# Optimization experiments

Measured on AMD Instinct MI355X. Metric: run time of the kernel, lower is better.

The kernel has to match this reference:

```python
import jax, jax.numpy as jnp
import numpy as np

D_MODEL = 1024
HEAD_SIZE = 64

def setup_inputs() -> dict:
    key = jax.random.key(0)
    ks = jax.random.split(key, 7)
    s = 1.0 / np.sqrt(D_MODEL)
    x = jax.random.normal(ks[0], (4, 4096, D_MODEL), dtype=jnp.float32)
    Wq = jax.random.uniform(ks[1], (D_MODEL, HEAD_SIZE), jnp.float32, -s, s)
    bq = jax.random.uniform(ks[2], (HEAD_SIZE,), jnp.float32, -s, s)
    Wk = jax.random.uniform(ks[3], (D_MODEL, HEAD_SIZE), jnp.float32, -s, s)
    bk = jax.random.uniform(ks[4], (HEAD_SIZE,), jnp.float32, -s, s)
    Wv = jax.random.uniform(ks[5], (D_MODEL, HEAD_SIZE), jnp.float32, -s, s)
    bv = jax.random.uniform(ks[6], (HEAD_SIZE,), jnp.float32, -s, s)
    return {"x": x, "Wq": Wq, "bq": bq, "Wk": Wk, "bk": bk, "Wv": Wv, "bv": bv}

def reference(x, Wq, bq, Wk, bk, Wv, bv):
    # x: [B, S, D]; projections to [B, S, H]
    Q = jnp.einsum('bsd,dh->bsh', x, Wq) + bq
    K = jnp.einsum('bsd,dh->bsh', x, Wk) + bk
    V = jnp.einsum('bsd,dh->bsh', x, Wv) + bv
    scores = jnp.einsum('bqh,bkh->bqk', Q, K) / jnp.sqrt(jnp.float32(HEAD_SIZE))
    attn = jax.nn.softmax(scores, axis=-1)  # [B, S, S]
    return jnp.einsum('bqk,bkh->bqh', attn, V)
```

## Files before the change

kernel.cpp:

```cpp
#include <hip/hip_runtime.h>
#include <hip/hip_bf16.h>


#define S_LEN 4096
#define D_MODEL 1024

typedef __attribute__((ext_vector_type(8))) short bf16x8;
typedef __attribute__((ext_vector_type(4))) float f32x4;
typedef __attribute__((ext_vector_type(16))) float f32x16;

__device__ inline short f2bf(float f) {
    union { float f; unsigned u; } v;
    v.f = f;
    unsigned r = v.u + 0x7fffu + ((v.u >> 16) & 1u);
    return (short)(r >> 16);
}

__device__ inline unsigned cvt_pk(float lo, float hi) {
    unsigned r;
    asm("v_cvt_pk_bf16_f32 %0, %1, %2" : "=v"(r) : "v"(lo), "v"(hi));
    return r;
}

__device__ inline void pl32swap(unsigned& a, unsigned& b) {
    asm("v_permlane32_swap_b32 %0, %1" : "+v"(a), "+v"(b));
}

__device__ inline f32x16 fzero16() {
    f32x16 z;
#pragma unroll
    for (int i = 0; i < 16; ++i) z[i] = 0.f;
    return z;
}

__device__ inline void gload_lds16(const void* g, void* l) {
    __builtin_amdgcn_global_load_lds((const __attribute__((address_space(1))) void*)g,
                                     (__attribute__((address_space(3))) void*)l, 16, 0, 0);
}

__global__ void prep_w(const float* __restrict__ Wq, const float* __restrict__ Wk,
                       const float* __restrict__ Wv, short* __restrict__ WtF) {
    int idx = blockIdx.x * 256 + threadIdx.x;
    int j = idx & 7;
    int lane = (idx >> 3) & 63;
    int f = idx >> 9;
    int ntg = f % 12;
    int kb = f / 12;
    int k = (kb >> 1) * 64 + (kb & 1) * 32 + (lane >> 4) * 8 + j;
    int c = ntg * 16 + (lane & 15);
    const float* W = (c < 64) ? Wq : (c < 128 ? Wk : Wv);
    WtF[idx] = f2bf(W[k * 64 + (c & 63)]);
}

__launch_bounds__(512)
__global__ void proj_kernel(const float* __restrict__ x, const short* __restrict__ WtF,
                            const float* __restrict__ bq, const float* __restrict__ bk,
                            const float* __restrict__ bv,
                            short* __restrict__ Qb, short* __restrict__ Kb,
                            short* __restrict__ Vt) {
    __shared__ __align__(16) char smem[73728];
    const float CEXP = 0.18033688011112042f;
    int w = threadIdx.x >> 6;
    int lane = threadIdx.x & 63;
    int g = lane >> 4, ln = lane & 15;
    int rt = w >> 2, nh = w & 3;
    int rowbase = blockIdx.x * 32;

    char* xbuf = smem;
    char* wbuf = smem + 24576;
    const char* xB = (const char*)x;
    const char* WtB = (const char*)WtF;

    auto stageX = [&](int buf, int bkt) {
        int od = w * 1024 + lane * 16;
        int row = od >> 8, col = od & 255;
        const char* src = xB + (size_t)(rowbase + row) * 4096 + bkt * 256
                          + (col ^ ((row & 7) << 5));
        gload_lds16(src, xbuf + buf * 8192 + w * 1024);
    };
    auto stageW = [&](int buf, int bkt) {
#pragma unroll
        for (int i = 0; i < 3; ++i) {
            const char* src = WtB + (size_t)bkt * 24576 + w * 3072 + i * 1024 + lane * 16;
            gload_lds16(src, wbuf + buf * 24576 + w * 3072 + i * 1024);
        }
    };

    f32x4 acc[3];
#pragma unroll
    for (int i = 0; i < 3; ++i) acc[i] = (f32x4){0.f, 0.f, 0.f, 0.f};

    stageX(0, 0);
    stageW(0, 0);
    stageX(1, 1);

    int arow = rt * 16 + ln;
    int aswz = (arow & 7) << 5;

#pragma unroll 1
    for (int t = 0; t < 16; ++t) {
        asm volatile("s_waitcnt vmcnt(1)" ::: "memory");
        __builtin_amdgcn_s_barrier();
        __builtin_amdgcn_sched_barrier(0);
        {
            int tn1 = t + 1 > 15 ? 15 : t + 1;
            int tn2 = t + 2 > 15 ? 15 : t + 2;
            stageW((t + 1) & 1, tn1);
            int xs = t + 2; while (xs >= 3) xs -= 3;
            stageX(xs, tn2);
        }
        int xj = t; while (xj >= 3) xj -= 3;
        const char* xc = xbuf + xj * 8192;
        const char* wc = wbuf + (t & 1) * 24576;

#pragma unroll
        for (int kk = 0; kk < 2; ++kk) {
            int cb = (kk * 128 + g * 32) ^ aswz;
            f32x4 X0 = *(const f32x4*)(xc + arow * 256 + cb);
            f32x4 X1 = *(const f32x4*)(xc + arow * 256 + cb + 16);
            union { bf16x8 v; unsigned u[4]; } A;
            A.u[0] = cvt_pk(X0[0], X0[1]);
            A.u[1] = cvt_pk(X0[2], X0[3]);
            A.u[2] = cvt_pk(X1[0], X1[1]);
            A.u[3] = cvt_pk(X1[2], X1[3]);
#pragma unroll
            for (int j = 0; j < 3; ++j) {
                int fr = kk * 12 + nh * 3 + j;
                bf16x8 bfr = *(const bf16x8*)(wc + fr * 1024 + lane * 16);
                acc[j] = __builtin_amdgcn_mfma_f32_16x16x32_bf16(A.v, bfr, acc[j], 0, 0, 0);
            }
        }
    }

    __syncthreads();
    short* vsm = (short*)smem;
#pragma unroll
    for (int j = 0; j < 3; ++j) {
        int ntg = nh * 3 + j;
        int c = ntg * 16 + ln;
        int proj = ntg >> 2;
        int h = c & 63;
        float bias = (proj == 0 ? bq : (proj == 1 ? bk : bv))[h];
#pragma unroll
        for (int r = 0; r < 4; ++r) {
            int srow = rowbase + rt * 16 + g * 4 + r;
            float v = acc[j][r] + bias;
            if (proj == 0) v *= CEXP;
            short hv = f2bf(v);
            if (proj == 0) {
                Qb[(size_t)srow * 64 + h] = hv;
            } else if (proj == 1) {
                Kb[(size_t)srow * 64 + h] = hv;
            } else {
                vsm[h * 36 + rt * 16 + g * 4 + r] = hv;
            }
        }
    }
    __syncthreads();
    {
        int t = threadIdx.x;
        int h = t >> 3, c = t & 7;
        uint2 val = *(const uint2*)(vsm + h * 36 + c * 4);
        int bb = rowbase >> 12;
        int sg = (rowbase & 4095) + c * 4;
        *(uint2*)(Vt + (((size_t)(bb * 64 + h)) << 12) + sg) = val;
    }
}

__launch_bounds__(512)
__global__ void attn_kernel(const short* __restrict__ Qb, const short* __restrict__ Kb,
                            const short* __restrict__ Vt, float* __restrict__ out) {
    __shared__ __align__(16) char smraw[131072];
    __shared__ float lsm[256];
    int lane = threadIdx.x & 63;
    int w = threadIdx.x >> 6;
    int l31 = lane & 31, hi = lane >> 5;
    int sp = w >> 1, qt = w & 1;

    int bid = blockIdx.x;
    int sb = (bid & 7) * 32 + (bid >> 3);
    int b = sb >> 6, qs = sb & 63;
    size_t qrow0 = ((size_t)b << 12) + (size_t)qs * 64;

    char* base = smraw + sp * 32768;
    char* kbuf = base;
    char* vbuf = base + 16384;

    const char* KB = (const char*)(Kb + (((size_t)b << 12) + sp * 1024) * 64);
    const char* VB = (const char*)Vt + (((size_t)b * 64) << 13) + (size_t)sp * 2048;

    auto stageT = [&](int buf, int t) {
        if (qt == 0) {
            char* dst = kbuf + buf * 8192;
#pragma unroll
            for (int i = 0; i < 8; ++i) {
                int od = i * 1024 + lane * 16;
                int row = od >> 7, colb = od & 127;
                const char* src = KB + (size_t)(t * 64 + row) * 128 + (colb ^ ((row & 7) << 4));
                gload_lds16(src, dst + i * 1024);
            }
        } else {
            char* dst = vbuf + buf * 8192;
#pragma unroll
            for (int i = 0; i < 8; ++i) {
                int od = i * 1024 + lane * 16;
                int row = od >> 7, colb = od & 127;
                const char* src = VB + (size_t)row * 8192 + t * 128 + (colb ^ ((row & 7) << 4));
                gload_lds16(src, dst + i * 1024);
            }
        }
    };

    bf16x8 qf[4];
    {
        const short* qp = Qb + (qrow0 + qt * 32 + l31) * 64 + hi * 8;
#pragma unroll
        for (int ks = 0; ks < 4; ++ks) qf[ks] = *(const bf16x8*)(qp + ks * 16);
    }

    f32x16 oacc0 = fzero16(), oacc1 = fzero16();
    float lacc[16];
#pragma unroll
    for (int r = 0; r < 16; ++r) lacc[r] = 0.f;

    int swz = (l31 & 7) << 4;
    stageT(0, 0);

#pragma unroll 1
    for (int t = 0; t < 16; ++t) {
        asm volatile("s_waitcnt vmcnt(0)" ::: "memory");
        __builtin_amdgcn_s_barrier();
        __builtin_amdgcn_sched_barrier(0);
        if (t < 15) stageT((t + 1) & 1, t + 1);

        const char* kc = kbuf + (t & 1) * 8192;
        const char* vc = vbuf + (t & 1) * 8192;

        bf16x8 kf[8];
#pragma unroll
        for (int kt = 0; kt < 2; ++kt)
#pragma unroll
            for (int ks = 0; ks < 4; ++ks)
                kf[kt * 4 + ks] = *(const bf16x8*)(kc + (kt * 32 + l31) * 128
                                                  + ((ks * 32 + hi * 16) ^ swz));
        f32x16 s0 = fzero16(), s1 = fzero16();
#pragma unroll
        for (int ks = 0; ks < 4; ++ks) {
            s0 = __builtin_amdgcn_mfma_f32_32x32x16_bf16(kf[ks], qf[ks], s0, 0, 0, 0);
            s1 = __builtin_amdgcn_mfma_f32_32x32x16_bf16(kf[4 + ks], qf[ks], s1, 0, 0, 0);
        }

        bf16x8 vf[8];
#pragma unroll
        for (int ht = 0; ht < 2; ++ht)
#pragma unroll
            for (int kk = 0; kk < 4; ++kk)
                vf[ht * 4 + kk] = *(const bf16x8*)(vc + (ht * 32 + l31) * 128
                                                   + ((kk * 32 + hi * 16) ^ swz));

        float p0[16], p1[16];
#pragma unroll
        for (int r = 0; r < 16; ++r) p0[r] = exp2f(s0[r]);
#pragma unroll
        for (int r = 0; r < 16; ++r) p1[r] = exp2f(s1[r]);
#pragma unroll
        for (int r = 0; r < 16; ++r) lacc[r] += p0[r] + p1[r];

        union { unsigned u[4]; bf16x8 v; } t00, t01, t10, t11;
        {
            unsigned D[8];
#pragma unroll
            for (int dw = 0; dw < 8; ++dw) D[dw] = cvt_pk(p0[2 * dw], p0[2 * dw + 1]);
            pl32swap(D[0], D[2]); pl32swap(D[1], D[3]);
            pl32swap(D[4], D[6]); pl32swap(D[5], D[7]);
            t00.u[0] = D[0]; t00.u[1] = D[1]; t00.u[2] = D[2]; t00.u[3] = D[3];
            t01.u[0] = D[4]; t01.u[1] = D[5]; t01.u[2] = D[6]; t01.u[3] = D[7];
        }
        {
            unsigned D[8];
#pragma unroll
            for (int dw = 0; dw < 8; ++dw) D[dw] = cvt_pk(p1[2 * dw], p1[2 * dw + 1]);
            pl32swap(D[0], D[2]); pl32swap(D[1], D[3]);
            pl32swap(D[4], D[6]); pl32swap(D[5], D[7]);
            t10.u[0] = D[0]; t10.u[1] = D[1]; t10.u[2] = D[2]; t10.u[3] = D[3];
            t11.u[0] = D[4]; t11.u[1] = D[5]; t11.u[2] = D[6]; t11.u[3] = D[7];
        }

        oacc0 = __builtin_amdgcn_mfma_f32_32x32x16_bf16(vf[0], t00.v, oacc0, 0, 0, 0);
        oacc1 = __builtin_amdgcn_mfma_f32_32x32x16_bf16(vf[4], t00.v, oacc1, 0, 0, 0);
        oacc0 = __builtin_amdgcn_mfma_f32_32x32x16_bf16(vf[1], t01.v, oacc0, 0, 0, 0);
        oacc1 = __builtin_amdgcn_mfma_f32_32x32x16_bf16(vf[5], t01.v, oacc1, 0, 0, 0);
        oacc0 = __builtin_amdgcn_mfma_f32_32x32x16_bf16(vf[2], t10.v, oacc0, 0, 0, 0);
        oacc1 = __builtin_amdgcn_mfma_f32_32x32x16_bf16(vf[6], t10.v, oacc1, 0, 0, 0);
        oacc0 = __builtin_amdgcn_mfma_f32_32x32x16_bf16(vf[3], t11.v, oacc0, 0, 0, 0);
        oacc1 = __builtin_amdgcn_mfma_f32_32x32x16_bf16(vf[7], t11.v, oacc1, 0, 0, 0);
    }

    float lfin;
    {
        float lt[8];
#pragma unroll
        for (int r = 0; r < 8; ++r) lt[r] = lacc[r] + lacc[r + 8];
#pragma unroll
        for (int st = 4; st >= 1; st >>= 1)
#pragma unroll
            for (int r = 0; r < 4; ++r)
                if (r < st) lt[r] += lt[r + st];
        lfin = lt[0] + __shfl_xor(lt[0], 32);
    }

    __syncthreads();
    float* osm = (float*)smraw;
    {
        float* ow = osm + (size_t)(w * 32 + l31) * 68;
#pragma unroll
        for (int r = 0; r < 16; ++r) {
            int h = (r & 3) + 8 * (r >> 2) + 4 * hi;
            ow[h] = oacc0[r];
            ow[32 + h] = oacc1[r];
        }
        if (hi == 0) lsm[w * 32 + l31] = lfin;
    }
    __syncthreads();
    {
        int tq = threadIdx.x >> 3, hb = (threadIdx.x & 7) * 8;
        int qt2 = tq >> 5, ql = tq & 31;
        f32x4 oa = (f32x4){0.f, 0.f, 0.f, 0.f}, ob = (f32x4){0.f, 0.f, 0.f, 0.f};
        float lsum = 0.f;
#pragma unroll
        for (int sp2 = 0; sp2 < 4; ++sp2) {
            int w2 = sp2 * 2 + qt2;
            lsum += lsm[w2 * 32 + ql];
            const float* src = osm + (size_t)(w2 * 32 + ql) * 68 + hb;
            f32x4 x0 = *(const f32x4*)src;
            f32x4 x1 = *(const f32x4*)(src + 4);
#pragma unroll
            for (int j = 0; j < 4; ++j) { oa[j] += x0[j]; ob[j] += x1[j]; }
        }
        float inv = 1.f / lsum;
        f32x4 r0, r1;
#pragma unroll
        for (int j = 0; j < 4; ++j) { r0[j] = oa[j] * inv; r1[j] = ob[j] * inv; }
        float* op = out + (qrow0 + tq) * 64 + hb;
        *(f32x4*)op = r0;
        *(f32x4*)(op + 4) = r1;
    }
}

extern "C" void kernel_launch(void* const* d_in, const int* in_sizes, int n_in,
                              void* d_out, int out_size, void* d_ws, size_t ws_size,
                              hipStream_t stream) {
    const float* x  = (const float*)d_in[0];
    const float* Wq = (const float*)d_in[1];
    const float* bq = (const float*)d_in[2];
    const float* Wk = (const float*)d_in[3];
    const float* bk = (const float*)d_in[4];
    const float* Wv = (const float*)d_in[5];
    const float* bv = (const float*)d_in[6];

    short* ws = (short*)d_ws;
    short* WtF = ws;
    short* Qb = WtF + 192 * 1024;
    short* Kb = Qb + 16384 * 64;
    short* Vt = Kb + 16384 * 64;

    prep_w<<<768, 256, 0, stream>>>(Wq, Wk, Wv, WtF);
    proj_kernel<<<512, 512, 0, stream>>>(x, WtF, bq, bk, bv, Qb, Kb, Vt);
    attn_kernel<<<256, 512, 0, stream>>>(Qb, Kb, Vt, (float*)d_out);
}
```

Measured before the change: 59.35 us.

## Split keys across all eight waves, each wave covering all 64 query rows

Waves no longer pair up as 4 key splits × 2 query tiles. Each of the 8 waves now takes its own 512-key slice and processes both 32-row query tiles, reusing its K and V fragments across the two. Each wave stages its own 32-key K and V tiles, so LDS reads per MFMA drop and the split of staging work between K and V waves goes away. The cost is doubled accumulator registers (four output tiles), a larger LDS reduction buffer, and an 8-way cross-wave sum at the end.

```diff
diff --git a/kernel.cpp b/kernel.cpp
--- a/kernel.cpp
+++ b/kernel.cpp
@@ -170,58 +170,63 @@
 __launch_bounds__(512)
 __global__ void attn_kernel(const short* __restrict__ Qb, const short* __restrict__ Kb,
                             const short* __restrict__ Vt, float* __restrict__ out) {
-    __shared__ __align__(16) char smraw[131072];
-    __shared__ float lsm[256];
+    __shared__ __align__(16) char smraw[139264];
+    __shared__ float lsm[512];
     int lane = threadIdx.x & 63;
     int w = threadIdx.x >> 6;
     int l31 = lane & 31, hi = lane >> 5;
-    int sp = w >> 1, qt = w & 1;
 
     int bid = blockIdx.x;
     int sb = (bid & 7) * 32 + (bid >> 3);
     int b = sb >> 6, qs = sb & 63;
     size_t qrow0 = ((size_t)b << 12) + (size_t)qs * 64;
 
-    char* base = smraw + sp * 32768;
+    char* base = smraw + w * 16384;
     char* kbuf = base;
-    char* vbuf = base + 16384;
-
-    const char* KB = (const char*)(Kb + (((size_t)b << 12) + sp * 1024) * 64);
-    const char* VB = (const char*)Vt + (((size_t)b * 64) << 13) + (size_t)sp * 2048;
+    char* vbuf = base + 8192;
+
+    const char* KB = (const char*)(Kb + (((size_t)b << 12) + w * 512) * 64);
+    const char* VB = (const char*)Vt + (((size_t)b * 64) << 13) + (size_t)w * 1024;
 
     auto stageT = [&](int buf, int t) {
-        if (qt == 0) {
-            char* dst = kbuf + buf * 8192;
-#pragma unroll
-            for (int i = 0; i < 8; ++i) {
+        {
+            char* dst = kbuf + buf * 4096;
+#pragma unroll
+            for (int i = 0; i < 4; ++i) {
                 int od = i * 1024 + lane * 16;
                 int row = od >> 7, colb = od & 127;
-                const char* src = KB + (size_t)(t * 64 + row) * 128 + (colb ^ ((row & 7) << 4));
+                const char* src = KB + (size_t)(t * 32 + row) * 128 + (colb ^ ((row & 7) << 4));
                 gload_lds16(src, dst + i * 1024);
             }
-        } else {
-            char* dst = vbuf + buf * 8192;
-#pragma unroll
-            for (int i = 0; i < 8; ++i) {
+        }
+        {
+            char* dst = vbuf + buf * 4096;
+#pragma unroll
+            for (int i = 0; i < 4; ++i) {
                 int od = i * 1024 + lane * 16;
-                int row = od >> 7, colb = od & 127;
-                const char* src = VB + (size_t)row * 8192 + t * 128 + (colb ^ ((row & 7) << 4));
+                int row = od >> 7;
+                int od2 = (od & 127) ^ ((row & 7) << 4);
+                int half = (od2 >> 6) & 1, colb = od2 & 63;
+                const char* src = VB + (size_t)(row + half * 32) * 8192 + t * 64 + colb;
                 gload_lds16(src, dst + i * 1024);
             }
         }
     };
 
-    bf16x8 qf[4];
+    bf16x8 qf0[4], qf1[4];
     {
-        const short* qp = Qb + (qrow0 + qt * 32 + l31) * 64 + hi * 8;
-#pragma unroll
-        for (int ks = 0; ks < 4; ++ks) qf[ks] = *(const bf16x8*)(qp + ks * 16);
-    }
-
-    f32x16 oacc0 = fzero16(), oacc1 = fzero16();
-    float lacc[16];
-#pragma unroll
-    for (int r = 0; r < 16; ++r) lacc[r] = 0.f;
+        const short* qp0 = Qb + (qrow0 + l31) * 64 + hi * 8;
+        const short* qp1 = Qb + (qrow0 + 32 + l31) * 64 + hi * 8;
+#pragma unroll
+        for (int ks = 0; ks < 4; ++ks) {
+            qf0[ks] = *(const bf16x8*)(qp0 + ks * 16);
+            qf1[ks] = *(const bf16x8*)(qp1 + ks * 16);
+        }
+    }
+
+    f32x16 oacc00 = fzero16(), oacc01 = fzero16();
+    f32x16 oacc10 = fzero16(), oacc11 = fzero16();
+    float lq0 = 0.f, lq1 = 0.f;
 
     int swz = (l31 & 7) << 4;
     stageT(0, 0);
@@ -233,105 +238,117 @@
         __builtin_amdgcn_sched_barrier(0);
         if (t < 15) stageT((t + 1) & 1, t + 1);
 
-        const char* kc = kbuf + (t & 1) * 8192;
-        const char* vc = vbuf + (t & 1) * 8192;
-
-        bf16x8 kf[8];
-#pragma unroll
-        for (int kt = 0; kt < 2; ++kt)
+        const char* kc = kbuf + (t & 1) * 4096;
+        const char* vc = vbuf + (t & 1) * 4096;
+
+        bf16x8 kf[4];
+#pragma unroll
+        for (int ks = 0; ks < 4; ++ks)
+            kf[ks] = *(const bf16x8*)(kc + l31 * 128 + ((ks * 32 + hi * 16) ^ swz));
+        bf16x8 vf[4];
+#pragma unroll
+        for (int ht = 0; ht < 2; ++ht)
+#pragma unroll
+            for (int ks2 = 0; ks2 < 2; ++ks2)
+                vf[ht * 2 + ks2] = *(const bf16x8*)(vc + l31 * 128
+                                    + ((ht * 64 + ks2 * 32 + hi * 16) ^ swz));
+
+        {
+            f32x16 s = fzero16();
 #pragma unroll
             for (int ks = 0; ks < 4; ++ks)
-                kf[kt * 4 + ks] = *(const bf16x8*)(kc + (kt * 32 + l31) * 128
-                                                  + ((ks * 32 + hi * 16) ^ swz));
-        f32x16 s0 = fzero16(), s1 = fzero16();
-#pragma unroll
-        for (int ks = 0; ks < 4; ++ks) {
-            s0 = __builtin_amdgcn_mfma_f32_32x32x16_bf16(kf[ks], qf[ks], s0, 0, 0, 0);
-            s1 = __builtin_amdgcn_mfma_f32_32x32x16_bf16(kf[4 + ks], qf[ks], s1, 0, 0, 0);
-        }
-
-        bf16x8 vf[8];
-#pragma unroll
-        for (int ht = 0; ht < 2; ++ht)
-#pragma unroll
-            for (int kk = 0; kk < 4; ++kk)
-                vf[ht * 4 + kk] = *(const bf16x8*)(vc + (ht * 32 + l31) * 128
-                                                   + ((kk * 32 + hi * 16) ^ swz));
-
-        float p0[16], p1[16];
-#pragma unroll
-        for (int r = 0; r < 16; ++r) p0[r] = exp2f(s0[r]);
-#pragma unroll
-        for (int r = 0; r < 16; ++r) p1[r] = exp2f(s1[r]);
-#pragma unroll
-        for (int r = 0; r < 16; ++r) lacc[r] += p0[r] + p1[r];
-
-        union { unsigned u[4]; bf16x8 v; } t00, t01, t10, t11;
-        {
+                s = __builtin_amdgcn_mfma_f32_32x32x16_bf16(kf[ks], qf0[ks], s, 0, 0, 0);
+            float p[16];
+#pragma unroll
+            for (int r = 0; r < 16; ++r) p[r] = exp2f(s[r]);
+            {
+                float sa[8];
+#pragma unroll
+                for (int r = 0; r < 8; ++r) sa[r] = p[r] + p[r + 8];
+#pragma unroll
+                for (int st = 4; st >= 1; st >>= 1)
+#pragma unroll
+                    for (int r = 0; r < 4; ++r)
+                        if (r < st) sa[r] += sa[r + st];
+                lq0 += sa[0];
+            }
             unsigned D[8];
 #pragma unroll
-            for (int dw = 0; dw < 8; ++dw) D[dw] = cvt_pk(p0[2 * dw], p0[2 * dw + 1]);
+            for (int dw = 0; dw < 8; ++dw) D[dw] = cvt_pk(p[2 * dw], p[2 * dw + 1]);
             pl32swap(D[0], D[2]); pl32swap(D[1], D[3]);
             pl32swap(D[4], D[6]); pl32swap(D[5], D[7]);
-            t00.u[0] = D[0]; t00.u[1] = D[1]; t00.u[2] = D[2]; t00.u[3] = D[3];
-            t01.u[0] = D[4]; t01.u[1] = D[5]; t01.u[2] = D[6]; t01.u[3] = D[7];
-        }
-        {
+            union { unsigned u[4]; bf16x8 v; } t0, t1;
+            t0.u[0] = D[0]; t0.u[1] = D[1]; t0.u[2] = D[2]; t0.u[3] = D[3];
+            t1.u[0] = D[4]; t1.u[1] = D[5]; t1.u[2] = D[6]; t1.u[3] = D[7];
+            oacc00 = __builtin_amdgcn_mfma_f32_32x32x16_bf16(vf[0], t0.v, oacc00, 0, 0, 0);
+            oacc01 = __builtin_amdgcn_mfma_f32_32x32x16_bf16(vf[2], t0.v, oacc01, 0, 0, 0);
+            oacc00 = __builtin_amdgcn_mfma_f32_32x32x16_bf16(vf[1], t1.v, oacc00, 0, 0, 0);
+            oacc01 = __builtin_amdgcn_mfma_f32_32x32x16_bf16(vf[3], t1.v, oacc01, 0, 0, 0);
+        }
+        {
+            f32x16 s = fzero16();
+#pragma unroll
+            for (int ks = 0; ks < 4; ++ks)
+                s = __builtin_amdgcn_mfma_f32_32x32x16_bf16(kf[ks], qf1[ks], s, 0, 0, 0);
+            float p[16];
+#pragma unroll
+            for (int r = 0; r < 16; ++r) p[r] = exp2f(s[r]);
+            {
+                float sa[8];
+#pragma unroll
+                for (int r = 0; r < 8; ++r) sa[r] = p[r] + p[r + 8];
+#pragma unroll
+                for (int st = 4; st >= 1; st >>= 1)
+#pragma unroll
+                    for (int r = 0; r < 4; ++r)
+                        if (r < st) sa[r] += sa[r + st];
+                lq1 += sa[0];
+            }
             unsigned D[8];
 #pragma unroll
-            for (int dw = 0; dw < 8; ++dw) D[dw] = cvt_pk(p1[2 * dw], p1[2 * dw + 1]);
+            for (int dw = 0; dw < 8; ++dw) D[dw] = cvt_pk(p[2 * dw], p[2 * dw + 1]);
             pl32swap(D[0], D[2]); pl32swap(D[1], D[3]);
             pl32swap(D[4], D[6]); pl32swap(D[5], D[7]);
-            t10.u[0] = D[0]; t10.u[1] = D[1]; t10.u[2] = D[2]; t10.u[3] = D[3];
-            t11.u[0] = D[4]; t11.u[1] = D[5]; t11.u[2] = D[6]; t11.u[3] = D[7];
-        }
-
-        oacc0 = __builtin_amdgcn_mfma_f32_32x32x16_bf16(vf[0], t00.v, oacc0, 0, 0, 0);
-        oacc1 = __builtin_amdgcn_mfma_f32_32x32x16_bf16(vf[4], t00.v, oacc1, 0, 0, 0);
-        oacc0 = __builtin_amdgcn_mfma_f32_32x32x16_bf16(vf[1], t01.v, oacc0, 0, 0, 0);
-        oacc1 = __builtin_amdgcn_mfma_f32_32x32x16_bf16(vf[5], t01.v, oacc1, 0, 0, 0);
-        oacc0 = __builtin_amdgcn_mfma_f32_32x32x16_bf16(vf[2], t10.v, oacc0, 0, 0, 0);
-        oacc1 = __builtin_amdgcn_mfma_f32_32x32x16_bf16(vf[6], t10.v, oacc1, 0, 0, 0);
-        oacc0 = __builtin_amdgcn_mfma_f32_32x32x16_bf16(vf[3], t11.v, oacc0, 0, 0, 0);
-        oacc1 = __builtin_amdgcn_mfma_f32_32x32x16_bf16(vf[7], t11.v, oacc1, 0, 0, 0);
-    }
-
-    float lfin;
-    {
-        float lt[8];
-#pragma unroll
-        for (int r = 0; r < 8; ++r) lt[r] = lacc[r] + lacc[r + 8];
-#pragma unroll
-        for (int st = 4; st >= 1; st >>= 1)
-#pragma unroll
-            for (int r = 0; r < 4; ++r)
-                if (r < st) lt[r] += lt[r + st];
-        lfin = lt[0] + __shfl_xor(lt[0], 32);
-    }
+            union { unsigned u[4]; bf16x8 v; } t0, t1;
+            t0.u[0] = D[0]; t0.u[1] = D[1]; t0.u[2] = D[2]; t0.u[3] = D[3];
+            t1.u[0] = D[4]; t1.u[1] = D[5]; t1.u[2] = D[6]; t1.u[3] = D[7];
+            oacc10 = __builtin_amdgcn_mfma_f32_32x32x16_bf16(vf[0], t0.v, oacc10, 0, 0, 0);
+            oacc11 = __builtin_amdgcn_mfma_f32_32x32x16_bf16(vf[2], t0.v, oacc11, 0, 0, 0);
+            oacc10 = __builtin_amdgcn_mfma_f32_32x32x16_bf16(vf[1], t1.v, oacc10, 0, 0, 0);
+            oacc11 = __builtin_amdgcn_mfma_f32_32x32x16_bf16(vf[3], t1.v, oacc11, 0, 0, 0);
+        }
+    }
+
+    float lf0 = lq0 + __shfl_xor(lq0, 32);
+    float lf1 = lq1 + __shfl_xor(lq1, 32);
 
     __syncthreads();
     float* osm = (float*)smraw;
     {
-        float* ow = osm + (size_t)(w * 32 + l31) * 68;
+        float* ow0 = osm + (size_t)(w * 64 + l31) * 68;
+        float* ow1 = osm + (size_t)(w * 64 + 32 + l31) * 68;
 #pragma unroll
         for (int r = 0; r < 16; ++r) {
             int h = (r & 3) + 8 * (r >> 2) + 4 * hi;
-            ow[h] = oacc0[r];
-            ow[32 + h] = oacc1[r];
-        }
-        if (hi == 0) lsm[w * 32 + l31] = lfin;
+            ow0[h] = oacc00[r];
+            ow0[32 + h] = oacc01[r];
+            ow1[h] = oacc10[r];
+            ow1[32 + h] = oacc11[r];
+        }
+        if (hi == 0) {
+            lsm[w * 64 + l31] = lf0;
+            lsm[w * 64 + 32 + l31] = lf1;
+        }
     }
     __syncthreads();
     {
         int tq = threadIdx.x >> 3, hb = (threadIdx.x & 7) * 8;
-        int qt2 = tq >> 5, ql = tq & 31;
         f32x4 oa = (f32x4){0.f, 0.f, 0.f, 0.f}, ob = (f32x4){0.f, 0.f, 0.f, 0.f};
         float lsum = 0.f;
 #pragma unroll
-        for (int sp2 = 0; sp2 < 4; ++sp2) {
-            int w2 = sp2 * 2 + qt2;
-            lsum += lsm[w2 * 32 + ql];
-            const float* src = osm + (size_t)(w2 * 32 + ql) * 68 + hb;
+        for (int w2 = 0; w2 < 8; ++w2) {
+            lsum += lsm[w2 * 64 + tq];
+            const float* src = osm + (size_t)(w2 * 64 + tq) * 68 + hb;
             f32x4 x0 = *(const f32x4*)src;
             f32x4 x1 = *(const f32x4*)(src + 4);
 #pragma unroll
```

New measurement: 65.41 us. 1.1x slower.
